# Kernel optimization log

Hardware: AMD Instinct MI355X
Metric: run time of the kernel (lower is better)

Reference implementation:

```python
import jax, jax.numpy as jnp
import numpy as np

N, K, M, DIM = 131072, 16, 128, 64


def setup_inputs() -> dict:
    key = jax.random.key(0)
    kx, ks, ka, kb = jax.random.split(key, 4)
    return {
        "x": jax.random.normal(kx, (N, DIM), dtype=jnp.float32),
        "s": jax.random.normal(ks, (K,), dtype=jnp.float32),
        "a": jax.random.normal(ka, (K, M, DIM), dtype=jnp.float32),
        "b": jax.random.normal(kb, (K, M), dtype=jnp.float32),
    }


def reference(x, s, a, b):
    # scores[k, n, m] = x[n, :] @ a[k, m, :] + b[k, m]  (batched GEMM over k)
    scores = jnp.einsum("nd,kmd->knm", x, a) + b[:, None, :]
    # per-expert logsumexp over the m affine pieces -> [k, n]
    lse = jax.nn.logsumexp(scores, axis=-1)
    # signed sum over experts -> [n]
    return jnp.einsum("k,kn->n", s, lse)
```

## Files before the change

### kernel.cpp

```cpp
#include <hip/hip_runtime.h>
#include <hip/hip_bf16.h>

#define NROWS 131072
#define KEXP 16
#define MPC 128
#define DIMD 64

typedef float f32x4 __attribute__((ext_vector_type(4)));
typedef short s16x8 __attribute__((ext_vector_type(8)));

#define L2E 1.4426950408889634f
#define LN2 0.6931471805599453f

static __device__ inline unsigned int b2u(__hip_bfloat162 h) {
    union { __hip_bfloat162 h; unsigned int u; } c;
    c.h = h;
    return c.u;
}

__global__ void prep_kernel(const float* __restrict__ a, const float* __restrict__ b,
                            short* __restrict__ abf, float* __restrict__ eb) {
    if (blockIdx.x < 128) {
        int i = (blockIdx.x * 256 + threadIdx.x) * 4;
        float4 v = *(const float4*)(a + i);
        __hip_bfloat162 p0 = __float22bfloat162_rn(make_float2(v.x * L2E, v.y * L2E));
        __hip_bfloat162 p1 = __float22bfloat162_rn(make_float2(v.z * L2E, v.w * L2E));
        uint2 u;
        u.x = b2u(p0);
        u.y = b2u(p1);
        *(uint2*)(abf + i) = u;
    } else {
        for (int r = threadIdx.x; r < KEXP * MPC; r += 256)
            eb[r] = __expf(b[r]);
    }
}

__global__ __launch_bounds__(256, 3)
void moe_lse_kernel(const float* __restrict__ x, const float* __restrict__ s,
                    const short* __restrict__ abf, const float* __restrict__ ebp,
                    float* __restrict__ lsew) {
    __shared__ int4 xbuf[1024];
    __shared__ float partial[4][128];

    const int tid  = threadIdx.x;
    const int w    = tid >> 6;
    const int l    = tid & 63;
    const int li   = l & 15;
    const int quad = l >> 4;

    const int eg     = blockIdx.x & 3;
    const int rb     = blockIdx.x >> 2;
    const int k      = eg * 4 + w;
    const int r_base = rb * 128;

    s16x8 Bf[16];
#pragma unroll
    for (int t = 0; t < 8; ++t) {
        const short* p = abf + ((k * MPC + t * 16 + li) * DIMD + quad * 8);
        Bf[t * 2 + 0] = *(const s16x8*)(p);
        Bf[t * 2 + 1] = *(const s16x8*)(p + 32);
    }
    float eb[8];
#pragma unroll
    for (int t = 0; t < 8; ++t) eb[t] = ebp[k * MPC + t * 16 + li];
    const float sk2 = s[k] * LN2;

#pragma unroll
    for (int i = 0; i < 4; ++i) {
        const int e   = i * 256 + tid;
        const int g   = e >> 7;
        const int dc  = (e >> 6) & 1;
        const int ll  = e & 63;
        const int sli = ll & 15;
        const int sq  = ll >> 4;
        const float* gp = x + (r_base + g * 16 + sli) * DIMD + dc * 32 + sq * 8;
        float4 f0 = *(const float4*)(gp);
        float4 f1 = *(const float4*)(gp + 4);
        __hip_bfloat162 p0 = __float22bfloat162_rn(make_float2(f0.x, f0.y));
        __hip_bfloat162 p1 = __float22bfloat162_rn(make_float2(f0.z, f0.w));
        __hip_bfloat162 p2 = __float22bfloat162_rn(make_float2(f1.x, f1.y));
        __hip_bfloat162 p3 = __float22bfloat162_rn(make_float2(f1.z, f1.w));
        int4 pk;
        pk.x = (int)b2u(p0); pk.y = (int)b2u(p1); pk.z = (int)b2u(p2); pk.w = (int)b2u(p3);
        xbuf[e] = pk;
    }
    __syncthreads();

    for (int g = 0; g < 8; ++g) {
        const short* xsp = (const short*)xbuf + g * 1024;
        s16x8 a0 = *(const s16x8*)(xsp + l * 8);
        s16x8 a1 = *(const s16x8*)(xsp + 512 + l * 8);

        f32x4 acc[8];
#pragma unroll
        for (int t = 0; t < 8; ++t) {
            f32x4 z = {0.f, 0.f, 0.f, 0.f};
            acc[t] = __builtin_amdgcn_mfma_f32_16x16x32_bf16(a0, Bf[t * 2 + 0], z, 0, 0, 0);
            acc[t] = __builtin_amdgcn_mfma_f32_16x16x32_bf16(a1, Bf[t * 2 + 1], acc[t], 0, 0, 0);
        }

        float sums[4];
#pragma unroll
        for (int j = 0; j < 4; ++j) {
            float sum = 0.f;
#pragma unroll
            for (int t = 0; t < 8; ++t)
                sum = fmaf(eb[t], __builtin_amdgcn_exp2f(acc[t][j]), sum);
            sum += __shfl_xor(sum, 1);
            sum += __shfl_xor(sum, 2);
            sum += __shfl_xor(sum, 4);
            sum += __shfl_xor(sum, 8);
            sums[j] = sum;
        }
        const int m3 = li & 3;
        float v = sums[0];
        v = (m3 == 1) ? sums[1] : v;
        v = (m3 == 2) ? sums[2] : v;
        v = (m3 == 3) ? sums[3] : v;
        float r = sk2 * __log2f(v);
        if (li < 4) partial[w][g * 16 + quad * 4 + li] = r;
    }
    __syncthreads();

    if (tid < 128) {
        float sv = partial[0][tid] + partial[1][tid] + partial[2][tid] + partial[3][tid];
        lsew[eg * NROWS + r_base + tid] = sv;
    }
}

__global__ void combine_kernel(const float* __restrict__ lsew, float* __restrict__ out) {
    const int i = blockIdx.x * 256 + threadIdx.x;
    const f32x4* p = (const f32x4*)lsew;
    const int stride = NROWS / 4;
    f32x4 v = p[i] + p[stride + i] + p[2 * stride + i] + p[3 * stride + i];
    ((f32x4*)out)[i] = v;
}

extern "C" void kernel_launch(void* const* d_in, const int* in_sizes, int n_in,
                              void* d_out, int out_size, void* d_ws, size_t ws_size,
                              hipStream_t stream) {
    const float* x = (const float*)d_in[0];
    const float* s = (const float*)d_in[1];
    const float* a = (const float*)d_in[2];
    const float* b = (const float*)d_in[3];
    float* out = (float*)d_out;

    short* abf  = (short*)d_ws;
    float* eb   = (float*)((char*)d_ws + (size_t)KEXP * MPC * DIMD * 2);
    float* lsew = (float*)((char*)d_ws + 264 * 1024);

    prep_kernel<<<129, 256, 0, stream>>>(a, b, abf, eb);

    const int rowblocks = NROWS / 128;
    moe_lse_kernel<<<rowblocks * 4, 256, 0, stream>>>(x, s, abf, eb, lsew);

    combine_kernel<<<NROWS / 1024, 256, 0, stream>>>(lsew, out);
}
```

Baseline: 127.7 us.

## Fuse prep, expert-group loop and combine into a single kernel

Replaces the three-kernel pipeline with one kernel. Each block now loops over all four expert groups for its 128 rows, converting fp32 weights to bf16 and computing exp(b) on the fly, and writes the final output directly. This removes two launches, the workspace round trip for partial sums, and the fourfold reload and conversion of x across expert-group blocks. In exchange each block re-reads and converts the fp32 weights four times, and the grid has a quarter as many blocks, which lowers parallelism.

```diff
diff --git a/kernel.cpp b/kernel.cpp
--- a/kernel.cpp
+++ b/kernel.cpp
@@ -18,27 +18,20 @@
     return c.u;
 }
 
-__global__ void prep_kernel(const float* __restrict__ a, const float* __restrict__ b,
-                            short* __restrict__ abf, float* __restrict__ eb) {
-    if (blockIdx.x < 128) {
-        int i = (blockIdx.x * 256 + threadIdx.x) * 4;
-        float4 v = *(const float4*)(a + i);
-        __hip_bfloat162 p0 = __float22bfloat162_rn(make_float2(v.x * L2E, v.y * L2E));
-        __hip_bfloat162 p1 = __float22bfloat162_rn(make_float2(v.z * L2E, v.w * L2E));
-        uint2 u;
-        u.x = b2u(p0);
-        u.y = b2u(p1);
-        *(uint2*)(abf + i) = u;
-    } else {
-        for (int r = threadIdx.x; r < KEXP * MPC; r += 256)
-            eb[r] = __expf(b[r]);
-    }
+static __device__ inline int4 cvt8(float4 f0, float4 f1, float sc) {
+    __hip_bfloat162 p0 = __float22bfloat162_rn(make_float2(f0.x * sc, f0.y * sc));
+    __hip_bfloat162 p1 = __float22bfloat162_rn(make_float2(f0.z * sc, f0.w * sc));
+    __hip_bfloat162 p2 = __float22bfloat162_rn(make_float2(f1.x * sc, f1.y * sc));
+    __hip_bfloat162 p3 = __float22bfloat162_rn(make_float2(f1.z * sc, f1.w * sc));
+    int4 pk;
+    pk.x = (int)b2u(p0); pk.y = (int)b2u(p1); pk.z = (int)b2u(p2); pk.w = (int)b2u(p3);
+    return pk;
 }
 
 __global__ __launch_bounds__(256, 3)
-void moe_lse_kernel(const float* __restrict__ x, const float* __restrict__ s,
-                    const short* __restrict__ abf, const float* __restrict__ ebp,
-                    float* __restrict__ lsew) {
+void fused_kernel(const float* __restrict__ x, const float* __restrict__ s,
+                  const float* __restrict__ a, const float* __restrict__ b,
+                  float* __restrict__ out) {
     __shared__ int4 xbuf[1024];
     __shared__ float partial[4][128];
 
@@ -48,22 +41,7 @@
     const int li   = l & 15;
     const int quad = l >> 4;
 
-    const int eg     = blockIdx.x & 3;
-    const int rb     = blockIdx.x >> 2;
-    const int k      = eg * 4 + w;
-    const int r_base = rb * 128;
-
-    s16x8 Bf[16];
-#pragma unroll
-    for (int t = 0; t < 8; ++t) {
-        const short* p = abf + ((k * MPC + t * 16 + li) * DIMD + quad * 8);
-        Bf[t * 2 + 0] = *(const s16x8*)(p);
-        Bf[t * 2 + 1] = *(const s16x8*)(p + 32);
-    }
-    float eb[8];
-#pragma unroll
-    for (int t = 0; t < 8; ++t) eb[t] = ebp[k * MPC + t * 16 + li];
-    const float sk2 = s[k] * LN2;
+    const int r_base = blockIdx.x * 128;
 
 #pragma unroll
     for (int i = 0; i < 4; ++i) {
@@ -76,64 +54,77 @@
         const float* gp = x + (r_base + g * 16 + sli) * DIMD + dc * 32 + sq * 8;
         float4 f0 = *(const float4*)(gp);
         float4 f1 = *(const float4*)(gp + 4);
-        __hip_bfloat162 p0 = __float22bfloat162_rn(make_float2(f0.x, f0.y));
-        __hip_bfloat162 p1 = __float22bfloat162_rn(make_float2(f0.z, f0.w));
-        __hip_bfloat162 p2 = __float22bfloat162_rn(make_float2(f1.x, f1.y));
-        __hip_bfloat162 p3 = __float22bfloat162_rn(make_float2(f1.z, f1.w));
-        int4 pk;
-        pk.x = (int)b2u(p0); pk.y = (int)b2u(p1); pk.z = (int)b2u(p2); pk.w = (int)b2u(p3);
-        xbuf[e] = pk;
+        xbuf[e] = cvt8(f0, f1, 1.0f);
     }
     __syncthreads();
 
-    for (int g = 0; g < 8; ++g) {
-        const short* xsp = (const short*)xbuf + g * 1024;
-        s16x8 a0 = *(const s16x8*)(xsp + l * 8);
-        s16x8 a1 = *(const s16x8*)(xsp + 512 + l * 8);
+    float racc[8];
+#pragma unroll
+    for (int g = 0; g < 8; ++g) racc[g] = 0.f;
 
-        f32x4 acc[8];
+    for (int e = 0; e < 4; ++e) {
+        const int k = e * 4 + w;
+
+        union { int4 i; s16x8 v; } Bf[16];
 #pragma unroll
         for (int t = 0; t < 8; ++t) {
-            f32x4 z = {0.f, 0.f, 0.f, 0.f};
-            acc[t] = __builtin_amdgcn_mfma_f32_16x16x32_bf16(a0, Bf[t * 2 + 0], z, 0, 0, 0);
-            acc[t] = __builtin_amdgcn_mfma_f32_16x16x32_bf16(a1, Bf[t * 2 + 1], acc[t], 0, 0, 0);
+            const float* p = a + ((size_t)(k * MPC + t * 16 + li) * DIMD + quad * 8);
+            float4 f00 = *(const float4*)(p);
+            float4 f01 = *(const float4*)(p + 4);
+            float4 f10 = *(const float4*)(p + 32);
+            float4 f11 = *(const float4*)(p + 36);
+            Bf[t * 2 + 0].i = cvt8(f00, f01, L2E);
+            Bf[t * 2 + 1].i = cvt8(f10, f11, L2E);
         }
+        float eb[8];
+#pragma unroll
+        for (int t = 0; t < 8; ++t) eb[t] = __expf(b[k * MPC + t * 16 + li]);
+        const float sk2 = s[k] * LN2;
 
-        float sums[4];
+        for (int g = 0; g < 8; ++g) {
+            const short* xsp = (const short*)xbuf + g * 1024;
+            s16x8 a0 = *(const s16x8*)(xsp + l * 8);
+            s16x8 a1 = *(const s16x8*)(xsp + 512 + l * 8);
+
+            f32x4 acc[8];
 #pragma unroll
-        for (int j = 0; j < 4; ++j) {
-            float sum = 0.f;
+            for (int t = 0; t < 8; ++t) {
+                f32x4 z = {0.f, 0.f, 0.f, 0.f};
+                acc[t] = __builtin_amdgcn_mfma_f32_16x16x32_bf16(a0, Bf[t * 2 + 0].v, z, 0, 0, 0);
+                acc[t] = __builtin_amdgcn_mfma_f32_16x16x32_bf16(a1, Bf[t * 2 + 1].v, acc[t], 0, 0, 0);
+            }
+
+            float sums[4];
 #pragma unroll
-            for (int t = 0; t < 8; ++t)
-                sum = fmaf(eb[t], __builtin_amdgcn_exp2f(acc[t][j]), sum);
-            sum += __shfl_xor(sum, 1);
-            sum += __shfl_xor(sum, 2);
-            sum += __shfl_xor(sum, 4);
-            sum += __shfl_xor(sum, 8);
-            sums[j] = sum;
+            for (int j = 0; j < 4; ++j) {
+                float sum = 0.f;
+#pragma unroll
+                for (int t = 0; t < 8; ++t)
+                    sum = fmaf(eb[t], __builtin_amdgcn_exp2f(acc[t][j]), sum);
+                sum += __shfl_xor(sum, 1);
+                sum += __shfl_xor(sum, 2);
+                sum += __shfl_xor(sum, 4);
+                sum += __shfl_xor(sum, 8);
+                sums[j] = sum;
+            }
+            const int m3 = li & 3;
+            float v = sums[0];
+            v = (m3 == 1) ? sums[1] : v;
+            v = (m3 == 2) ? sums[2] : v;
+            v = (m3 == 3) ? sums[3] : v;
+            racc[g] += sk2 * __log2f(v);
         }
-        const int m3 = li & 3;
-        float v = sums[0];
-        v = (m3 == 1) ? sums[1] : v;
-        v = (m3 == 2) ? sums[2] : v;
-        v = (m3 == 3) ? sums[3] : v;
-        float r = sk2 * __log2f(v);
-        if (li < 4) partial[w][g * 16 + quad * 4 + li] = r;
     }
+
+#pragma unroll
+    for (int g = 0; g < 8; ++g)
+        if (li < 4) partial[w][g * 16 + quad * 4 + li] = racc[g];
     __syncthreads();
 
     if (tid < 128) {
-        float sv = partial[0][tid] + partial[1][tid] + partial[2][tid] + partial[3][tid];
-        lsew[eg * NROWS + r_base + tid] = sv;
+        out[r_base + tid] =
+            partial[0][tid] + partial[1][tid] + partial[2][tid] + partial[3][tid];
     }
-}
-
-__global__ void combine_kernel(const float* __restrict__ lsew, float* __restrict__ out) {
-    const int i = blockIdx.x * 256 + threadIdx.x;
-    const f32x4* p = (const f32x4*)lsew;
-    const int stride = NROWS / 4;
-    f32x4 v = p[i] + p[stride + i] + p[2 * stride + i] + p[3 * stride + i];
-    ((f32x4*)out)[i] = v;
 }
 
 extern "C" void kernel_launch(void* const* d_in, const int* in_sizes, int n_in,
@@ -145,14 +136,5 @@
     const float* b = (const float*)d_in[3];
     float* out = (float*)d_out;
 
-    short* abf  = (short*)d_ws;
-    float* eb   = (float*)((char*)d_ws + (size_t)KEXP * MPC * DIMD * 2);
-    float* lsew = (float*)((char*)d_ws + 264 * 1024);
-
-    prep_kernel<<<129, 256, 0, stream>>>(a, b, abf, eb);
-
-    const int rowblocks = NROWS / 128;
-    moe_lse_kernel<<<rowblocks * 4, 256, 0, stream>>>(x, s, abf, eb, lsew);
-
-    combine_kernel<<<NROWS / 1024, 256, 0, stream>>>(lsew, out);
+    fused_kernel<<<NROWS / 128, 256, 0, stream>>>(x, s, a, b, out);
 }
```

Result: slower. 214.5 us (+67.9%).

## Fuse all experts per row block into one kernel and drop combine pass

Applied to the files above, without the earlier changes.

Each 512-thread block now takes a 128-row tile and loops over all 16 experts, with each wave handling half of one expert's 128 pieces per pass. This removes the combine kernel, the intermediate lsew buffer and the fourfold re-reading and conversion of x. The bias is folded into the MFMA accumulator init in place of an exp(b) multiply, and the cross-lane reductions use DPP instead of shuffles. In exchange, B fragments are reloaded from global memory on every expert pass, and extra LDS is needed to combine the two half sums before the log.

```diff
diff --git a/kernel.cpp b/kernel.cpp
--- a/kernel.cpp
+++ b/kernel.cpp
@@ -12,34 +12,43 @@
 #define L2E 1.4426950408889634f
 #define LN2 0.6931471805599453f
 
+#define DPP_ADD(v, ctrl) \
+    ((v) + __int_as_float(__builtin_amdgcn_update_dpp( \
+         0, __float_as_int(v), (ctrl), 0xF, 0xF, true)))
+
 static __device__ inline unsigned int b2u(__hip_bfloat162 h) {
     union { __hip_bfloat162 h; unsigned int u; } c;
     c.h = h;
     return c.u;
 }
 
-__global__ void prep_kernel(const float* __restrict__ a, const float* __restrict__ b,
-                            short* __restrict__ abf, float* __restrict__ eb) {
-    if (blockIdx.x < 128) {
-        int i = (blockIdx.x * 256 + threadIdx.x) * 4;
-        float4 v = *(const float4*)(a + i);
-        __hip_bfloat162 p0 = __float22bfloat162_rn(make_float2(v.x * L2E, v.y * L2E));
-        __hip_bfloat162 p1 = __float22bfloat162_rn(make_float2(v.z * L2E, v.w * L2E));
-        uint2 u;
-        u.x = b2u(p0);
-        u.y = b2u(p1);
-        *(uint2*)(abf + i) = u;
-    } else {
-        for (int r = threadIdx.x; r < KEXP * MPC; r += 256)
-            eb[r] = __expf(b[r]);
-    }
+static __device__ inline int4 cvt8(float4 f0, float4 f1) {
+    __hip_bfloat162 p0 = __float22bfloat162_rn(make_float2(f0.x, f0.y));
+    __hip_bfloat162 p1 = __float22bfloat162_rn(make_float2(f0.z, f0.w));
+    __hip_bfloat162 p2 = __float22bfloat162_rn(make_float2(f1.x, f1.y));
+    __hip_bfloat162 p3 = __float22bfloat162_rn(make_float2(f1.z, f1.w));
+    int4 pk;
+    pk.x = (int)b2u(p0); pk.y = (int)b2u(p1); pk.z = (int)b2u(p2); pk.w = (int)b2u(p3);
+    return pk;
 }
 
-__global__ __launch_bounds__(256, 3)
-void moe_lse_kernel(const float* __restrict__ x, const float* __restrict__ s,
-                    const short* __restrict__ abf, const float* __restrict__ ebp,
-                    float* __restrict__ lsew) {
-    __shared__ int4 xbuf[1024];
+__global__ void prep_kernel(const float* __restrict__ a, short* __restrict__ abf) {
+    int i = (blockIdx.x * 256 + threadIdx.x) * 4;
+    float4 v = *(const float4*)(a + i);
+    __hip_bfloat162 p0 = __float22bfloat162_rn(make_float2(v.x * L2E, v.y * L2E));
+    __hip_bfloat162 p1 = __float22bfloat162_rn(make_float2(v.z * L2E, v.w * L2E));
+    uint2 u;
+    u.x = b2u(p0);
+    u.y = b2u(p1);
+    *(uint2*)(abf + i) = u;
+}
+
+__global__ __launch_bounds__(512, 4)
+void fused_kernel(const float* __restrict__ x, const float* __restrict__ s,
+                  const short* __restrict__ abf, const float* __restrict__ b,
+                  float* __restrict__ out) {
+    __shared__ int4  xbuf[1024];
+    __shared__ float hs[2][128][17];
     __shared__ float partial[4][128];
 
     const int tid  = threadIdx.x;
@@ -48,26 +57,11 @@
     const int li   = l & 15;
     const int quad = l >> 4;
 
-    const int eg     = blockIdx.x & 3;
-    const int rb     = blockIdx.x >> 2;
-    const int k      = eg * 4 + w;
-    const int r_base = rb * 128;
-
-    s16x8 Bf[16];
-#pragma unroll
-    for (int t = 0; t < 8; ++t) {
-        const short* p = abf + ((k * MPC + t * 16 + li) * DIMD + quad * 8);
-        Bf[t * 2 + 0] = *(const s16x8*)(p);
-        Bf[t * 2 + 1] = *(const s16x8*)(p + 32);
-    }
-    float eb[8];
-#pragma unroll
-    for (int t = 0; t < 8; ++t) eb[t] = ebp[k * MPC + t * 16 + li];
-    const float sk2 = s[k] * LN2;
+    const int r_base = blockIdx.x * 128;
 
 #pragma unroll
-    for (int i = 0; i < 4; ++i) {
-        const int e   = i * 256 + tid;
+    for (int i = 0; i < 2; ++i) {
+        const int e   = i * 512 + tid;
         const int g   = e >> 7;
         const int dc  = (e >> 6) & 1;
         const int ll  = e & 63;
@@ -76,64 +70,80 @@
         const float* gp = x + (r_base + g * 16 + sli) * DIMD + dc * 32 + sq * 8;
         float4 f0 = *(const float4*)(gp);
         float4 f1 = *(const float4*)(gp + 4);
-        __hip_bfloat162 p0 = __float22bfloat162_rn(make_float2(f0.x, f0.y));
-        __hip_bfloat162 p1 = __float22bfloat162_rn(make_float2(f0.z, f0.w));
-        __hip_bfloat162 p2 = __float22bfloat162_rn(make_float2(f1.x, f1.y));
-        __hip_bfloat162 p3 = __float22bfloat162_rn(make_float2(f1.z, f1.w));
-        int4 pk;
-        pk.x = (int)b2u(p0); pk.y = (int)b2u(p1); pk.z = (int)b2u(p2); pk.w = (int)b2u(p3);
-        xbuf[e] = pk;
+        xbuf[e] = cvt8(f0, f1);
     }
     __syncthreads();
 
-    for (int g = 0; g < 8; ++g) {
-        const short* xsp = (const short*)xbuf + g * 1024;
-        s16x8 a0 = *(const s16x8*)(xsp + l * 8);
-        s16x8 a1 = *(const s16x8*)(xsp + 512 + l * 8);
+    for (int tt = 0; tt < 4; ++tt) {
+        const int id = tt * 8 + w;
+        const int k  = id & 15;
+        const int h  = id >> 4;
 
-        f32x4 acc[8];
+        s16x8 Bf[8];
 #pragma unroll
-        for (int t = 0; t < 8; ++t) {
-            f32x4 z = {0.f, 0.f, 0.f, 0.f};
-            acc[t] = __builtin_amdgcn_mfma_f32_16x16x32_bf16(a0, Bf[t * 2 + 0], z, 0, 0, 0);
-            acc[t] = __builtin_amdgcn_mfma_f32_16x16x32_bf16(a1, Bf[t * 2 + 1], acc[t], 0, 0, 0);
+        for (int t = 0; t < 4; ++t) {
+            const short* p = abf + ((k * MPC + h * 64 + t * 16 + li) * DIMD + quad * 8);
+            Bf[t * 2 + 0] = *(const s16x8*)(p);
+            Bf[t * 2 + 1] = *(const s16x8*)(p + 32);
         }
+        float lb[4];
+#pragma unroll
+        for (int t = 0; t < 4; ++t)
+            lb[t] = b[k * MPC + h * 64 + t * 16 + li] * L2E;
 
-        float sums[4];
+        for (int g = 0; g < 8; ++g) {
+            const short* xsp = (const short*)xbuf + g * 1024;
+            s16x8 a0 = *(const s16x8*)(xsp + l * 8);
+            s16x8 a1 = *(const s16x8*)(xsp + 512 + l * 8);
+
+            f32x4 acc[4];
 #pragma unroll
-        for (int j = 0; j < 4; ++j) {
-            float sum = 0.f;
+            for (int t = 0; t < 4; ++t) {
+                f32x4 c = {lb[t], lb[t], lb[t], lb[t]};
+                acc[t] = __builtin_amdgcn_mfma_f32_16x16x32_bf16(a0, Bf[t * 2 + 0], c, 0, 0, 0);
+                acc[t] = __builtin_amdgcn_mfma_f32_16x16x32_bf16(a1, Bf[t * 2 + 1], acc[t], 0, 0, 0);
+            }
+
+            float sums[4];
 #pragma unroll
-            for (int t = 0; t < 8; ++t)
-                sum = fmaf(eb[t], __builtin_amdgcn_exp2f(acc[t][j]), sum);
-            sum += __shfl_xor(sum, 1);
-            sum += __shfl_xor(sum, 2);
-            sum += __shfl_xor(sum, 4);
-            sum += __shfl_xor(sum, 8);
-            sums[j] = sum;
+            for (int j = 0; j < 4; ++j) {
+                float s01 = __builtin_amdgcn_exp2f(acc[0][j]) + __builtin_amdgcn_exp2f(acc[1][j]);
+                float s23 = __builtin_amdgcn_exp2f(acc[2][j]) + __builtin_amdgcn_exp2f(acc[3][j]);
+                float sum = s01 + s23;
+                sum = DPP_ADD(sum, 0xB1);
+                sum = DPP_ADD(sum, 0x4E);
+                sum = DPP_ADD(sum, 0x141);
+                sum = DPP_ADD(sum, 0x140);
+                sums[j] = sum;
+            }
+            const int m3 = li & 3;
+            float v = sums[0];
+            v = (m3 == 1) ? sums[1] : v;
+            v = (m3 == 2) ? sums[2] : v;
+            v = (m3 == 3) ? sums[3] : v;
+            if (li < 4) hs[h][g * 16 + quad * 4 + li][k] = v;
         }
-        const int m3 = li & 3;
-        float v = sums[0];
-        v = (m3 == 1) ? sums[1] : v;
-        v = (m3 == 2) ? sums[2] : v;
-        v = (m3 == 3) ? sums[3] : v;
-        float r = sk2 * __log2f(v);
-        if (li < 4) partial[w][g * 16 + quad * 4 + li] = r;
+    }
+    __syncthreads();
+
+    {
+        const int r    = tid & 127;
+        const int ksub = tid >> 7;
+        float acc2 = 0.f;
+#pragma unroll
+        for (int e = 0; e < 4; ++e) {
+            const int k = ksub * 4 + e;
+            float tot = hs[0][r][k] + hs[1][r][k];
+            acc2 = fmaf(s[k] * LN2, __log2f(tot), acc2);
+        }
+        partial[ksub][r] = acc2;
     }
     __syncthreads();
 
     if (tid < 128) {
-        float sv = partial[0][tid] + partial[1][tid] + partial[2][tid] + partial[3][tid];
-        lsew[eg * NROWS + r_base + tid] = sv;
+        out[r_base + tid] =
+            partial[0][tid] + partial[1][tid] + partial[2][tid] + partial[3][tid];
     }
-}
-
-__global__ void combine_kernel(const float* __restrict__ lsew, float* __restrict__ out) {
-    const int i = blockIdx.x * 256 + threadIdx.x;
-    const f32x4* p = (const f32x4*)lsew;
-    const int stride = NROWS / 4;
-    f32x4 v = p[i] + p[stride + i] + p[2 * stride + i] + p[3 * stride + i];
-    ((f32x4*)out)[i] = v;
 }
 
 extern "C" void kernel_launch(void* const* d_in, const int* in_sizes, int n_in,
@@ -145,14 +155,8 @@
     const float* b = (const float*)d_in[3];
     float* out = (float*)d_out;
 
-    short* abf  = (short*)d_ws;
-    float* eb   = (float*)((char*)d_ws + (size_t)KEXP * MPC * DIMD * 2);
-    float* lsew = (float*)((char*)d_ws + 264 * 1024);
+    short* abf = (short*)d_ws;
 
-    prep_kernel<<<129, 256, 0, stream>>>(a, b, abf, eb);
-
-    const int rowblocks = NROWS / 128;
-    moe_lse_kernel<<<rowblocks * 4, 256, 0, stream>>>(x, s, abf, eb, lsew);
-
-    combine_kernel<<<NROWS / 1024, 256, 0, stream>>>(lsew, out);
+    prep_kernel<<<(KEXP * MPC * DIMD) / 1024, 256, 0, stream>>>(a, abf);
+    fused_kernel<<<NROWS / 128, 512, 0, stream>>>(x, s, abf, b, out);
 }
```

Measured after the change: 137.8 us. 1.08x slower.
